# Kernel tuning notes

Hardware: AMD Instinct MI355X
Metric: run time of the kernel (lower is better)

The kernel has to match this reference:

```python
import jax, jax.numpy as jnp
import numpy as np

EPS = 1e-5

def _binarize(x):
    # binarize11: map to {-1, +1}
    return jnp.where(x >= 0, 1.0, -1.0).astype(x.dtype)

def _batchnorm(h, g, b):
    # training-mode BatchNorm1D over batch dim
    m = jnp.mean(h, axis=0)
    v = jnp.var(h, axis=0)
    return g * (h - m) * jax.lax.rsqrt(v + EPS) + b


def setup_inputs() -> dict:
    key = jax.random.key(0)
    ks = jax.random.split(key, 6)
    B = 32768
    dims = [(256, 784), (256, 256), (256, 256), (256, 256), (10, 256)]
    inp = {"x": jax.random.uniform(ks[0], (B, 784), dtype=jnp.float32)}
    for i, (o, iN) in enumerate(dims):
        inp[f"W{i}"] = jax.random.normal(ks[i + 1], (o, iN), dtype=jnp.float32)
        inp[f"g{i}"] = jnp.ones((o,), dtype=jnp.float32)
        inp[f"b{i}"] = jnp.zeros((o,), dtype=jnp.float32)
    return inp


def reference(x, W0, W1, W2, W3, W4, g0, g1, g2, g3, g4, b0, b1, b2, b3, b4):
    Ws = [W0, W1, W2, W3, W4]
    gs = [g0, g1, g2, g3, g4]
    bs = [b0, b1, b2, b3, b4]
    out = x - 0.5
    for k in range(5):
        a = _binarize(out)            # [B, in] in {-1,+1}
        wb = _binarize(Ws[k])         # [out, in] in {-1,+1}
        h = a @ wb.T                  # binary-weight linear
        out = _batchnorm(h, gs[k], bs[k])
    return jax.nn.softmax(out, axis=1)
```

## Files before the change

### kernel.cpp

```cpp
#include <hip/hip_runtime.h>
#include <stdint.h>


typedef unsigned long long u64;

#define NREP 16

#define OFF_WB0   0u
#define OFF_WB1   32768u
#define OFF_WB2   40960u
#define OFF_WB3   49152u
#define OFF_WB4   57344u
#define OFF_SUMD  57856u
#define OFF_SUMDD 139776u
#define STATS_INT4 15360
#define OFF_A1    (1u<<20)
#define OFF_A2    (2u<<20)
#define OFF_A3    (3u<<20)
#define OFF_A4    (4u<<20)
#define OFF_H0    (5u<<20)

__device__ __forceinline__ u64 pack784_sel(const float* __restrict__ src,
                                           float thr, int lane) {
  u64 w[13];
  const float4* s4 = (const float4*)src;
#pragma unroll
  for (int j = 0; j < 3; ++j) {
    float4 v = s4[j * 64 + lane];
    w[4*j+0] = __ballot(v.x >= thr);
    w[4*j+1] = __ballot(v.y >= thr);
    w[4*j+2] = __ballot(v.z >= thr);
    w[4*j+3] = __ballot(v.w >= thr);
  }
  float4 v = make_float4(-1.f, -1.f, -1.f, -1.f);
  if (lane < 4) v = s4[192 + lane];
  u64 m0 = __ballot(v.x >= thr) & 0xFull;
  u64 m1 = __ballot(v.y >= thr) & 0xFull;
  u64 m2 = __ballot(v.z >= thr) & 0xFull;
  u64 m3 = __ballot(v.w >= thr) & 0xFull;
  w[12] = m0 | (m1 << 4) | (m2 << 8) | (m3 << 12);
  u64 sel = 0;
#pragma unroll
  for (int i = 0; i < 13; ++i) sel = (lane == i) ? w[i] : sel;
  return sel;
}

__device__ __forceinline__ u64 pack256_sel(const float* __restrict__ src, int lane) {
  u64 w[4];
#pragma unroll
  for (int j = 0; j < 4; ++j) w[j] = __ballot(src[j * 64 + lane] >= 0.0f);
  u64 sel = 0;
#pragma unroll
  for (int i = 0; i < 4; ++i) sel = (lane == i) ? w[i] : sel;
  return sel;
}

__device__ __forceinline__ void bn_gs_md(const int* __restrict__ sumd_rep,
                                         const u64* __restrict__ sumdd_rep,
                                         int layer, int col,
                                         const float* __restrict__ g,
                                         float& gs, float& md_out) {
  long long sd = 0; u64 sdd = 0;
#pragma unroll
  for (int r = 0; r < NREP; ++r) {
    sd  += sumd_rep [(r * 5 + layer) * 256 + col];
    sdd += sumdd_rep[(r * 5 + layer) * 256 + col];
  }
  double md  = (double)sd  * (1.0 / 32768.0);
  double mdd = (double)sdd * (1.0 / 32768.0);
  float var = (float)(4.0 * (mdd - md * md));
  float s   = rsqrtf(var + 1e-5f);
  gs = g[col] * s;
  md_out = (float)md;
}

__global__ __launch_bounds__(256) void pack_weights(
    const float* __restrict__ W0, const float* __restrict__ W1,
    const float* __restrict__ W2, const float* __restrict__ W3,
    const float* __restrict__ W4,
    u64* __restrict__ wb0, u64* __restrict__ wb1, u64* __restrict__ wb2,
    u64* __restrict__ wb3, u64* __restrict__ wb4, int4* __restrict__ statsZ) {
  const int b = blockIdx.x, tid = threadIdx.x;
  const int lane = tid & 63, wave = tid >> 6;
  int gid = b * 256 + tid;
  if (gid < STATS_INT4) statsZ[gid] = make_int4(0, 0, 0, 0);
  if (b < 64) {
    int row = b * 4 + wave;
    u64 sel = pack784_sel(W0 + (size_t)row * 784, 0.0f, lane);
    if (lane < 13) wb0[lane * 256 + row] = sel;
  } else if (b < 128) {
    int row = (b - 64) * 4 + wave;
    u64 sel = pack256_sel(W1 + (size_t)row * 256, lane);
    if (lane < 4) wb1[lane * 256 + row] = sel;
  } else if (b < 192) {
    int row = (b - 128) * 4 + wave;
    u64 sel = pack256_sel(W2 + (size_t)row * 256, lane);
    if (lane < 4) wb2[lane * 256 + row] = sel;
  } else if (b < 256) {
    int row = (b - 192) * 4 + wave;
    u64 sel = pack256_sel(W3 + (size_t)row * 256, lane);
    if (lane < 4) wb3[lane * 256 + row] = sel;
  } else {
    for (int row = wave; row < 10; row += 4) {
      u64 sel = pack256_sel(W4 + (size_t)row * 256, lane);
      if (lane < 4) wb4[lane * 16 + row] = sel;
    }
  }
}

__global__ __launch_bounds__(256, 3) void mm0_kernel(
    const float* __restrict__ x, const u64* __restrict__ wb0T,
    short* __restrict__ h0, int* __restrict__ sumd_rep, u64* __restrict__ sumdd_rep) {
  const int b = blockIdx.x, tid = threadIdx.x;
  const int lane = tid & 63, wave = tid >> 6;
  const int row0 = b * 16;
  __shared__ u64 a0T[16 * 16];
  u64 w0  = wb0T[ 0 * 256 + tid], w1  = wb0T[ 1 * 256 + tid];
  u64 w2  = wb0T[ 2 * 256 + tid], w3  = wb0T[ 3 * 256 + tid];
  u64 w4  = wb0T[ 4 * 256 + tid], w5  = wb0T[ 5 * 256 + tid];
  u64 w6  = wb0T[ 6 * 256 + tid], w7  = wb0T[ 7 * 256 + tid];
  u64 w8  = wb0T[ 8 * 256 + tid], w9  = wb0T[ 9 * 256 + tid];
  u64 w10 = wb0T[10 * 256 + tid], w11 = wb0T[11 * 256 + tid];
  u64 w12 = wb0T[12 * 256 + tid];
  {
    const float* base = x + (size_t)(row0 + wave * 4) * 784;
#pragma unroll
    for (int it = 0; it < 4; ++it) {
      u64 sel = pack784_sel(base + (size_t)it * 784, 0.5f, lane);
      if (lane < 16) a0T[(wave * 4 + it) * 16 + lane] = sel;
    }
  }
  __syncthreads();
  int sd = 0; unsigned sdd = 0;
#pragma unroll 4
  for (int r = 0; r < 16; ++r) {
    const u64* ap = &a0T[r * 16];
    int d = __popcll(ap[0] ^ w0)   + __popcll(ap[1] ^ w1)
          + __popcll(ap[2] ^ w2)   + __popcll(ap[3] ^ w3)
          + __popcll(ap[4] ^ w4)   + __popcll(ap[5] ^ w5)
          + __popcll(ap[6] ^ w6)   + __popcll(ap[7] ^ w7)
          + __popcll(ap[8] ^ w8)   + __popcll(ap[9] ^ w9)
          + __popcll(ap[10] ^ w10) + __popcll(ap[11] ^ w11)
          + __popcll(ap[12] ^ w12);
    h0[(size_t)(row0 + r) * 256 + tid] = (short)(784 - 2 * d);
    sd += d; sdd += (unsigned)(d * d);
  }
  const int rep = b & (NREP - 1);
  atomicAdd(&sumd_rep [(rep * 5 + 0) * 256 + tid], sd);
  atomicAdd(&sumdd_rep[(rep * 5 + 0) * 256 + tid], (u64)sdd);
}

__global__ __launch_bounds__(256, 4) void b0_kernel(
    const short* __restrict__ h0,
    int* __restrict__ sumd_rep, u64* __restrict__ sumdd_rep,
    const float* __restrict__ g0, const float* __restrict__ bb0,
    u64* __restrict__ a1, const u64* __restrict__ wb1T) {
  const int b = blockIdx.x, tid = threadIdx.x;
  const int lane = tid & 63, wave = tid >> 6;
  const int row0 = b * 32;
  float gs, md;
  bn_gs_md(sumd_rep, sumdd_rep, 0, tid, g0, gs, md);
  const float mh = 784.0f - 2.0f * md;
  const float bb = bb0[tid];
  u64 wn0 = wb1T[0 * 256 + tid], wn1 = wb1T[1 * 256 + tid];
  u64 wn2 = wb1T[2 * 256 + tid], wn3 = wb1T[3 * 256 + tid];
  __shared__ u64 bits[32 * 4];
#pragma unroll 8
  for (int r = 0; r < 32; ++r) {
    float hv = (float)h0[(size_t)(row0 + r) * 256 + tid];
    bool bit = fmaf(gs, hv - mh, bb) >= 0.0f;
    u64 m = __ballot(bit);
    if (lane == 0) bits[r * 4 + wave] = m;
  }
  __syncthreads();
  if (tid < 128) a1[(size_t)row0 * 4 + tid] = bits[tid];
  int sd = 0; unsigned sdd = 0;
#pragma unroll 8
  for (int r = 0; r < 32; ++r) {
    int d = __popcll(bits[r*4+0] ^ wn0) + __popcll(bits[r*4+1] ^ wn1)
          + __popcll(bits[r*4+2] ^ wn2) + __popcll(bits[r*4+3] ^ wn3);
    sd += d; sdd += (unsigned)(d * d);
  }
  const int rep = b & (NREP - 1);
  atomicAdd(&sumd_rep [(rep * 5 + 1) * 256 + tid], sd);
  atomicAdd(&sumdd_rep[(rep * 5 + 1) * 256 + tid], (u64)sdd);
}

template<int LAYER, int NNEXT, int NSTRIDE>
__global__ __launch_bounds__(256, 4) void bmid_kernel(
    const u64* __restrict__ aK, const u64* __restrict__ wbKT,
    int* __restrict__ sumd_rep, u64* __restrict__ sumdd_rep,
    const float* __restrict__ gK, const float* __restrict__ bK,
    u64* __restrict__ aN, const u64* __restrict__ wbNT) {
  const int b = blockIdx.x, tid = threadIdx.x;
  const int lane = tid & 63, wave = tid >> 6;
  const int row0 = b * 32;
  __shared__ u64 ain[32 * 4];
  __shared__ u64 bits[32 * 4];
  if (tid < 128) ain[tid] = aK[(size_t)row0 * 4 + tid];
  float gs, md;
  bn_gs_md(sumd_rep, sumdd_rep, LAYER, tid, gK, gs, md);
  const float A = -2.0f * gs;
  const float C = fmaf(gs, 2.0f * md, bK[tid]);
  u64 wk0 = wbKT[0 * 256 + tid], wk1 = wbKT[1 * 256 + tid];
  u64 wk2 = wbKT[2 * 256 + tid], wk3 = wbKT[3 * 256 + tid];
  __syncthreads();
#pragma unroll 8
  for (int r = 0; r < 32; ++r) {
    int d = __popcll(ain[r*4+0] ^ wk0) + __popcll(ain[r*4+1] ^ wk1)
          + __popcll(ain[r*4+2] ^ wk2) + __popcll(ain[r*4+3] ^ wk3);
    bool bit = fmaf(A, (float)d, C) >= 0.0f;
    u64 m = __ballot(bit);
    if (lane == 0) bits[r * 4 + wave] = m;
  }
  __syncthreads();
  if (tid < 128) aN[(size_t)row0 * 4 + tid] = bits[tid];
  if (tid < NNEXT) {
    u64 wn0 = wbNT[0 * NSTRIDE + tid], wn1 = wbNT[1 * NSTRIDE + tid];
    u64 wn2 = wbNT[2 * NSTRIDE + tid], wn3 = wbNT[3 * NSTRIDE + tid];
    int sd = 0; unsigned sdd = 0;
#pragma unroll 8
    for (int r = 0; r < 32; ++r) {
      int d = __popcll(bits[r*4+0] ^ wn0) + __popcll(bits[r*4+1] ^ wn1)
            + __popcll(bits[r*4+2] ^ wn2) + __popcll(bits[r*4+3] ^ wn3);
      sd += d; sdd += (unsigned)(d * d);
    }
    const int rep = b & (NREP - 1);
    atomicAdd(&sumd_rep [(rep * 5 + LAYER + 1) * 256 + tid], sd);
    atomicAdd(&sumdd_rep[(rep * 5 + LAYER + 1) * 256 + tid], (u64)sdd);
  }
}

__global__ __launch_bounds__(256) void b4_kernel(
    const u64* __restrict__ a4, const u64* __restrict__ wb4T,
    const int* __restrict__ sumd_rep, const u64* __restrict__ sumdd_rep,
    const float* __restrict__ g4, const float* __restrict__ bb4,
    float* __restrict__ out) {
  __shared__ float sA[10], sC[10];
  __shared__ u64 w4s[40];
  const int tid = threadIdx.x;
  if (tid < 40) w4s[tid] = wb4T[(tid & 3) * 16 + (tid >> 2)];
  if (tid < 10) {
    float gs, md;
    bn_gs_md(sumd_rep, sumdd_rep, 4, tid, g4, gs, md);
    sA[tid] = -2.0f * gs;
    sC[tid] = fmaf(gs, 2.0f * md, bb4[tid]);
  }
  __syncthreads();
  const int row = blockIdx.x * 256 + tid;
  u64 a[4];
#pragma unroll
  for (int i = 0; i < 4; ++i) a[i] = a4[(size_t)row * 4 + i];
  float y[10];
  float mx = -1e30f;
#pragma unroll
  for (int c = 0; c < 10; ++c) {
    int d = __popcll(a[0] ^ w4s[c*4+0]) + __popcll(a[1] ^ w4s[c*4+1])
          + __popcll(a[2] ^ w4s[c*4+2]) + __popcll(a[3] ^ w4s[c*4+3]);
    y[c] = fmaf(sA[c], (float)d, sC[c]);
    mx = fmaxf(mx, y[c]);
  }
  float sum = 0.0f;
#pragma unroll
  for (int c = 0; c < 10; ++c) { y[c] = __expf(y[c] - mx); sum += y[c]; }
  float inv = 1.0f / sum;
#pragma unroll
  for (int c = 0; c < 10; ++c) out[(size_t)row * 10 + c] = y[c] * inv;
}

extern "C" void kernel_launch(void* const* d_in, const int* in_sizes, int n_in,
                              void* d_out, int out_size, void* d_ws, size_t ws_size,
                              hipStream_t stream) {
  (void)in_sizes; (void)n_in; (void)out_size; (void)ws_size;
  const float* x   = (const float*)d_in[0];
  const float* W0  = (const float*)d_in[1];
  const float* g0  = (const float*)d_in[2];
  const float* bb0 = (const float*)d_in[3];
  const float* W1  = (const float*)d_in[4];
  const float* g1  = (const float*)d_in[5];
  const float* bb1 = (const float*)d_in[6];
  const float* W2  = (const float*)d_in[7];
  const float* g2  = (const float*)d_in[8];
  const float* bb2 = (const float*)d_in[9];
  const float* W3  = (const float*)d_in[10];
  const float* g3  = (const float*)d_in[11];
  const float* bb3 = (const float*)d_in[12];
  const float* W4  = (const float*)d_in[13];
  const float* g4  = (const float*)d_in[14];
  const float* bb4 = (const float*)d_in[15];

  char* ws = (char*)d_ws;
  u64*   wb0 = (u64*)(ws + OFF_WB0);
  u64*   wb1 = (u64*)(ws + OFF_WB1);
  u64*   wb2 = (u64*)(ws + OFF_WB2);
  u64*   wb3 = (u64*)(ws + OFF_WB3);
  u64*   wb4 = (u64*)(ws + OFF_WB4);
  int*   sumd  = (int*)(ws + OFF_SUMD);
  u64*   sumdd = (u64*)(ws + OFF_SUMDD);
  u64*   a1 = (u64*)(ws + OFF_A1);
  u64*   a2 = (u64*)(ws + OFF_A2);
  u64*   a3 = (u64*)(ws + OFF_A3);
  u64*   a4 = (u64*)(ws + OFF_A4);
  short* h0 = (short*)(ws + OFF_H0);

  pack_weights<<<257, 256, 0, stream>>>(W0, W1, W2, W3, W4,
                                        wb0, wb1, wb2, wb3, wb4,
                                        (int4*)(ws + OFF_SUMD));
  mm0_kernel<<<2048, 256, 0, stream>>>(x, wb0, h0, sumd, sumdd);
  b0_kernel<<<1024, 256, 0, stream>>>(h0, sumd, sumdd, g0, bb0, a1, wb1);
  bmid_kernel<1, 256, 256><<<1024, 256, 0, stream>>>(a1, wb1, sumd, sumdd, g1, bb1, a2, wb2);
  bmid_kernel<2, 256, 256><<<1024, 256, 0, stream>>>(a2, wb2, sumd, sumdd, g2, bb2, a3, wb3);
  bmid_kernel<3, 10, 16><<<1024, 256, 0, stream>>>(a3, wb3, sumd, sumdd, g3, bb3, a4, wb4);
  b4_kernel<<<128, 256, 0, stream>>>(a4, wb4, sumd, sumdd, g4, bb4, (float*)d_out);
}
```

Baseline: 254.9 us.

## Fuse all BNN layers into one cooperative persistent kernel with grid syncs

Replaces the seven-kernel chain with a single cooperative kernel of 512 blocks, each owning 64 batch rows. Per-row popcount results stay in registers (packed 16-bit) across layers, so the intermediate activation buffers and their global traffic go away. Grid-wide syncs separate weight packing, each layer's batch-statistics accumulation, and the final softmax. The multi-kernel path is kept as a fallback if the cooperative launch fails. The risk is heavy register use under the occupancy bound needed for co-residency, and the cost of grid syncs.

```diff
diff --git a/kernel.cpp b/kernel.cpp
--- a/kernel.cpp
+++ b/kernel.cpp
@@ -1,7 +1,9 @@
 #include <hip/hip_runtime.h>
+#include <hip/hip_cooperative_groups.h>
 #include <stdint.h>
 
 
+namespace cg = cooperative_groups;
 typedef unsigned long long u64;
 
 #define NREP 16
@@ -72,6 +74,191 @@
   float s   = rsqrtf(var + 1e-5f);
   gs = g[col] * s;
   md_out = (float)md;
+}
+
+#define DPK_SET(r, d) do { if ((r) & 1) dpk[(r) >> 1] |= ((unsigned)(d)) << 16; \
+                           else dpk[(r) >> 1] = (unsigned)(d); } while (0)
+#define DPK_GET(r) ((int)((dpk[(r) >> 1] >> (((r) & 1) * 16)) & 0xFFFFu))
+
+__global__ __launch_bounds__(256, 3) void fused_bnn(
+    const float* __restrict__ x,
+    const float* __restrict__ W0, const float* __restrict__ W1,
+    const float* __restrict__ W2, const float* __restrict__ W3,
+    const float* __restrict__ W4,
+    const float* __restrict__ g0, const float* __restrict__ g1,
+    const float* __restrict__ g2, const float* __restrict__ g3,
+    const float* __restrict__ g4,
+    const float* __restrict__ bb0, const float* __restrict__ bb1,
+    const float* __restrict__ bb2, const float* __restrict__ bb3,
+    const float* __restrict__ bb4,
+    float* __restrict__ out, char* __restrict__ ws) {
+  cg::grid_group grid = cg::this_grid();
+
+  u64* wb0 = (u64*)(ws + OFF_WB0);
+  u64* wb1 = (u64*)(ws + OFF_WB1);
+  u64* wb2 = (u64*)(ws + OFF_WB2);
+  u64* wb3 = (u64*)(ws + OFF_WB3);
+  u64* wb4 = (u64*)(ws + OFF_WB4);
+  int* sumd  = (int*)(ws + OFF_SUMD);
+  u64* sumdd = (u64*)(ws + OFF_SUMDD);
+
+  const int b = blockIdx.x, tid = threadIdx.x;
+  const int lane = tid & 63, wave = tid >> 6;
+  const int row0 = b * 64;
+  const int rep = b & (NREP - 1);
+
+  __shared__ u64 aw[64 * 16];
+  __shared__ u64 bits[64 * 4];
+  __shared__ float sY[640];
+
+  unsigned dpk[32];
+
+  {
+    int gid = b * 256 + tid;
+    if (gid < STATS_INT4) ((int4*)(ws + OFF_SUMD))[gid] = make_int4(0, 0, 0, 0);
+    if (b < 64) {
+      int row = b * 4 + wave;
+      u64 sel = pack784_sel(W0 + (size_t)row * 784, 0.0f, lane);
+      if (lane < 13) wb0[lane * 256 + row] = sel;
+    } else if (b < 128) {
+      int row = (b - 64) * 4 + wave;
+      u64 sel = pack256_sel(W1 + (size_t)row * 256, lane);
+      if (lane < 4) wb1[lane * 256 + row] = sel;
+    } else if (b < 192) {
+      int row = (b - 128) * 4 + wave;
+      u64 sel = pack256_sel(W2 + (size_t)row * 256, lane);
+      if (lane < 4) wb2[lane * 256 + row] = sel;
+    } else if (b < 256) {
+      int row = (b - 192) * 4 + wave;
+      u64 sel = pack256_sel(W3 + (size_t)row * 256, lane);
+      if (lane < 4) wb3[lane * 256 + row] = sel;
+    } else if (b == 256) {
+      for (int row = wave; row < 10; row += 4) {
+        u64 sel = pack256_sel(W4 + (size_t)row * 256, lane);
+        if (lane < 4) wb4[lane * 16 + row] = sel;
+      }
+    }
+  }
+  grid.sync();
+
+  {
+    u64 w0  = wb0[ 0 * 256 + tid], w1  = wb0[ 1 * 256 + tid];
+    u64 w2  = wb0[ 2 * 256 + tid], w3  = wb0[ 3 * 256 + tid];
+    u64 w4  = wb0[ 4 * 256 + tid], w5  = wb0[ 5 * 256 + tid];
+    u64 w6  = wb0[ 6 * 256 + tid], w7  = wb0[ 7 * 256 + tid];
+    u64 w8  = wb0[ 8 * 256 + tid], w9  = wb0[ 9 * 256 + tid];
+    u64 w10 = wb0[10 * 256 + tid], w11 = wb0[11 * 256 + tid];
+    u64 w12 = wb0[12 * 256 + tid];
+    const float* base = x + (size_t)(row0 + wave * 16) * 784;
+#pragma unroll 2
+    for (int it = 0; it < 16; ++it) {
+      u64 sel = pack784_sel(base + (size_t)it * 784, 0.5f, lane);
+      if (lane < 13) aw[(wave * 16 + it) * 16 + lane] = sel;
+    }
+    __syncthreads();
+    int sd = 0; unsigned sdd = 0;
+#pragma unroll
+    for (int r = 0; r < 64; ++r) {
+      const u64* ap = &aw[r * 16];
+      int d = __popcll(ap[0] ^ w0)   + __popcll(ap[1] ^ w1)
+            + __popcll(ap[2] ^ w2)   + __popcll(ap[3] ^ w3)
+            + __popcll(ap[4] ^ w4)   + __popcll(ap[5] ^ w5)
+            + __popcll(ap[6] ^ w6)   + __popcll(ap[7] ^ w7)
+            + __popcll(ap[8] ^ w8)   + __popcll(ap[9] ^ w9)
+            + __popcll(ap[10] ^ w10) + __popcll(ap[11] ^ w11)
+            + __popcll(ap[12] ^ w12);
+      DPK_SET(r, d);
+      sd += d; sdd += (unsigned)(d * d);
+    }
+    atomicAdd(&sumd [(rep * 5 + 0) * 256 + tid], sd);
+    atomicAdd(&sumdd[(rep * 5 + 0) * 256 + tid], (u64)sdd);
+  }
+  grid.sync();
+
+#pragma unroll
+  for (int k = 0; k < 3; ++k) {
+    const float* gk  = (k == 0) ? g0  : (k == 1) ? g1  : g2;
+    const float* bk  = (k == 0) ? bb0 : (k == 1) ? bb1 : bb2;
+    const u64*   wbN = (k == 0) ? wb1 : (k == 1) ? wb2 : wb3;
+    float gs, md;
+    bn_gs_md(sumd, sumdd, k, tid, gk, gs, md);
+    const float A = -2.0f * gs;
+    const float C = fmaf(gs, 2.0f * md, bk[tid]);
+#pragma unroll
+    for (int r = 0; r < 64; ++r) {
+      bool bit = fmaf(A, (float)DPK_GET(r), C) >= 0.0f;
+      u64 m = __ballot(bit);
+      if (lane == 0) bits[r * 4 + wave] = m;
+    }
+    __syncthreads();
+    u64 wn0 = wbN[0 * 256 + tid], wn1 = wbN[1 * 256 + tid];
+    u64 wn2 = wbN[2 * 256 + tid], wn3 = wbN[3 * 256 + tid];
+    int sd = 0; unsigned sdd = 0;
+#pragma unroll
+    for (int r = 0; r < 64; ++r) {
+      int d = __popcll(bits[r*4+0] ^ wn0) + __popcll(bits[r*4+1] ^ wn1)
+            + __popcll(bits[r*4+2] ^ wn2) + __popcll(bits[r*4+3] ^ wn3);
+      DPK_SET(r, d);
+      sd += d; sdd += (unsigned)(d * d);
+    }
+    atomicAdd(&sumd [(rep * 5 + k + 1) * 256 + tid], sd);
+    atomicAdd(&sumdd[(rep * 5 + k + 1) * 256 + tid], (u64)sdd);
+    grid.sync();
+  }
+
+  {
+    float gs, md;
+    bn_gs_md(sumd, sumdd, 3, tid, g3, gs, md);
+    const float A = -2.0f * gs;
+    const float C = fmaf(gs, 2.0f * md, bb3[tid]);
+#pragma unroll
+    for (int r = 0; r < 64; ++r) {
+      bool bit = fmaf(A, (float)DPK_GET(r), C) >= 0.0f;
+      u64 m = __ballot(bit);
+      if (lane == 0) bits[r * 4 + wave] = m;
+    }
+    __syncthreads();
+    if (tid < 10) {
+      u64 wn0 = wb4[0 * 16 + tid], wn1 = wb4[1 * 16 + tid];
+      u64 wn2 = wb4[2 * 16 + tid], wn3 = wb4[3 * 16 + tid];
+      int sd = 0; unsigned sdd = 0;
+#pragma unroll
+      for (int r = 0; r < 64; ++r) {
+        int d = __popcll(bits[r*4+0] ^ wn0) + __popcll(bits[r*4+1] ^ wn1)
+              + __popcll(bits[r*4+2] ^ wn2) + __popcll(bits[r*4+3] ^ wn3);
+        DPK_SET(r, d);
+        sd += d; sdd += (unsigned)(d * d);
+      }
+      atomicAdd(&sumd [(rep * 5 + 4) * 256 + tid], sd);
+      atomicAdd(&sumdd[(rep * 5 + 4) * 256 + tid], (u64)sdd);
+    }
+  }
+  grid.sync();
+
+  {
+    if (tid < 10) {
+      float gs, md;
+      bn_gs_md(sumd, sumdd, 4, tid, g4, gs, md);
+      const float A = -2.0f * gs;
+      const float C = fmaf(gs, 2.0f * md, bb4[tid]);
+#pragma unroll
+      for (int r = 0; r < 64; ++r)
+        sY[r * 10 + tid] = fmaf(A, (float)DPK_GET(r), C);
+    }
+    __syncthreads();
+    if (tid < 64) {
+      float y[10]; float mx = -1e30f;
+#pragma unroll
+      for (int c = 0; c < 10; ++c) { y[c] = sY[tid * 10 + c]; mx = fmaxf(mx, y[c]); }
+      float sum = 0.0f;
+#pragma unroll
+      for (int c = 0; c < 10; ++c) { y[c] = __expf(y[c] - mx); sum += y[c]; }
+      float inv = 1.0f / sum;
+      float* op = out + (size_t)(row0 + tid) * 10;
+#pragma unroll
+      for (int c = 0; c < 10; ++c) op[c] = y[c] * inv;
+    }
+  }
 }
 
 __global__ __launch_bounds__(256) void pack_weights(
@@ -288,28 +475,38 @@
   const float* W4  = (const float*)d_in[13];
   const float* g4  = (const float*)d_in[14];
   const float* bb4 = (const float*)d_in[15];
-
+  float* outp = (float*)d_out;
   char* ws = (char*)d_ws;
-  u64*   wb0 = (u64*)(ws + OFF_WB0);
-  u64*   wb1 = (u64*)(ws + OFF_WB1);
-  u64*   wb2 = (u64*)(ws + OFF_WB2);
-  u64*   wb3 = (u64*)(ws + OFF_WB3);
-  u64*   wb4 = (u64*)(ws + OFF_WB4);
-  int*   sumd  = (int*)(ws + OFF_SUMD);
-  u64*   sumdd = (u64*)(ws + OFF_SUMDD);
-  u64*   a1 = (u64*)(ws + OFF_A1);
-  u64*   a2 = (u64*)(ws + OFF_A2);
-  u64*   a3 = (u64*)(ws + OFF_A3);
-  u64*   a4 = (u64*)(ws + OFF_A4);
-  short* h0 = (short*)(ws + OFF_H0);
-
-  pack_weights<<<257, 256, 0, stream>>>(W0, W1, W2, W3, W4,
-                                        wb0, wb1, wb2, wb3, wb4,
-                                        (int4*)(ws + OFF_SUMD));
-  mm0_kernel<<<2048, 256, 0, stream>>>(x, wb0, h0, sumd, sumdd);
-  b0_kernel<<<1024, 256, 0, stream>>>(h0, sumd, sumdd, g0, bb0, a1, wb1);
-  bmid_kernel<1, 256, 256><<<1024, 256, 0, stream>>>(a1, wb1, sumd, sumdd, g1, bb1, a2, wb2);
-  bmid_kernel<2, 256, 256><<<1024, 256, 0, stream>>>(a2, wb2, sumd, sumdd, g2, bb2, a3, wb3);
-  bmid_kernel<3, 10, 16><<<1024, 256, 0, stream>>>(a3, wb3, sumd, sumdd, g3, bb3, a4, wb4);
-  b4_kernel<<<128, 256, 0, stream>>>(a4, wb4, sumd, sumdd, g4, bb4, (float*)d_out);
-}
+
+  void* args[] = { &x, &W0, &W1, &W2, &W3, &W4,
+                   &g0, &g1, &g2, &g3, &g4,
+                   &bb0, &bb1, &bb2, &bb3, &bb4,
+                   &outp, &ws };
+  hipError_t err = hipLaunchCooperativeKernel((const void*)fused_bnn,
+                                              dim3(512), dim3(256),
+                                              args, 0, stream);
+  if (err != hipSuccess) {
+    (void)hipGetLastError();
+    u64*   wb0 = (u64*)(ws + OFF_WB0);
+    u64*   wb1 = (u64*)(ws + OFF_WB1);
+    u64*   wb2 = (u64*)(ws + OFF_WB2);
+    u64*   wb3 = (u64*)(ws + OFF_WB3);
+    u64*   wb4 = (u64*)(ws + OFF_WB4);
+    int*   sumd  = (int*)(ws + OFF_SUMD);
+    u64*   sumdd = (u64*)(ws + OFF_SUMDD);
+    u64*   a1 = (u64*)(ws + OFF_A1);
+    u64*   a2 = (u64*)(ws + OFF_A2);
+    u64*   a3 = (u64*)(ws + OFF_A3);
+    u64*   a4 = (u64*)(ws + OFF_A4);
+    short* h0 = (short*)(ws + OFF_H0);
+    pack_weights<<<257, 256, 0, stream>>>(W0, W1, W2, W3, W4,
+                                          wb0, wb1, wb2, wb3, wb4,
+                                          (int4*)(ws + OFF_SUMD));
+    mm0_kernel<<<2048, 256, 0, stream>>>(x, wb0, h0, sumd, sumdd);
+    b0_kernel<<<1024, 256, 0, stream>>>(h0, sumd, sumdd, g0, bb0, a1, wb1);
+    bmid_kernel<1, 256, 256><<<1024, 256, 0, stream>>>(a1, wb1, sumd, sumdd, g1, bb1, a2, wb2);
+    bmid_kernel<2, 256, 256><<<1024, 256, 0, stream>>>(a2, wb2, sumd, sumdd, g2, bb2, a3, wb3);
+    bmid_kernel<3, 10, 16><<<1024, 256, 0, stream>>>(a3, wb3, sumd, sumdd, g3, bb3, a4, wb4);
+    b4_kernel<<<128, 256, 0, stream>>>(a4, wb4, sumd, sumdd, g4, bb4, (float*)d_out);
+  }
+}
```

After: 579.2 us. +127.2%, slower.

## Fuse all BNN layers into one persistent kernel with grid barriers

Applied to the files above, without the earlier changes.

Replaces the six per-layer kernels with a single persistent kernel of 512 blocks, each owning 64 rows. Per-row popcount results stay packed in registers across layers, so the intermediate h0 and activation bit arrays no longer go through global memory. BatchNorm statistics are synchronised with a hierarchical atomic grid barrier. In exchange it relies on all 512 blocks being co-resident, where a spin barrier could deadlock if they are not. It also raises register pressure, and the final layers leave most threads idle.

```diff
diff --git a/kernel.cpp b/kernel.cpp
--- a/kernel.cpp
+++ b/kernel.cpp
@@ -5,6 +5,9 @@
 typedef unsigned long long u64;
 
 #define NREP 16
+#define GRID_BLOCKS 512
+#define NGROUPS 32
+#define GROUP_SZ 16
 
 #define OFF_WB0   0u
 #define OFF_WB1   32768u
@@ -13,12 +16,8 @@
 #define OFF_WB4   57344u
 #define OFF_SUMD  57856u
 #define OFF_SUMDD 139776u
-#define STATS_INT4 15360
-#define OFF_A1    (1u<<20)
-#define OFF_A2    (2u<<20)
-#define OFF_A3    (3u<<20)
-#define OFF_A4    (4u<<20)
-#define OFF_H0    (5u<<20)
+#define OFF_BAR   303616u
+#define ZERO_INT4 16144
 
 __device__ __forceinline__ u64 pack784_sel(const float* __restrict__ src,
                                            float thr, int lane) {
@@ -63,8 +62,10 @@
   long long sd = 0; u64 sdd = 0;
 #pragma unroll
   for (int r = 0; r < NREP; ++r) {
-    sd  += sumd_rep [(r * 5 + layer) * 256 + col];
-    sdd += sumdd_rep[(r * 5 + layer) * 256 + col];
+    sd  += __hip_atomic_load(&sumd_rep [(r * 5 + layer) * 256 + col],
+                             __ATOMIC_RELAXED, __HIP_MEMORY_SCOPE_AGENT);
+    sdd += __hip_atomic_load(&sumdd_rep[(r * 5 + layer) * 256 + col],
+                             __ATOMIC_RELAXED, __HIP_MEMORY_SCOPE_AGENT);
   }
   double md  = (double)sd  * (1.0 / 32768.0);
   double mdd = (double)sdd * (1.0 / 32768.0);
@@ -74,16 +75,55 @@
   md_out = (float)md;
 }
 
+#define DPK_SET(r, d) do { if ((r) & 1) dpk[(r) >> 1] |= ((unsigned)(d)) << 16; \
+                           else dpk[(r) >> 1] = (unsigned)(d); } while (0)
+#define DPK_GET(r) ((int)((dpk[(r) >> 1] >> (((r) & 1) * 16)) & 0xFFFFu))
+
+__device__ __forceinline__ void stats_add(int* pd, u64* pdd, int sd, u64 sdd) {
+  int o1 = atomicAdd(pd, sd);
+  u64 o2 = atomicAdd(pdd, sdd);
+  asm volatile("" :: "v"(o1), "v"(o2));
+}
+
+__device__ __forceinline__ void grid_barrier(unsigned* bar, unsigned phase, int b) {
+  __syncthreads();
+  if (threadIdx.x == 0) {
+    asm volatile("s_waitcnt vmcnt(0)" ::: "memory");
+    const unsigned g = (unsigned)b >> 4;
+    unsigned a = __hip_atomic_fetch_add(&bar[g * 64], 1u, __ATOMIC_RELAXED,
+                                        __HIP_MEMORY_SCOPE_AGENT) + 1u;
+    bool released = false;
+    if (a == phase * GROUP_SZ) {
+      unsigned r = __hip_atomic_fetch_add(&bar[32 * 64], 1u, __ATOMIC_RELAXED,
+                                          __HIP_MEMORY_SCOPE_AGENT) + 1u;
+      if (r == phase * NGROUPS) {
+#pragma unroll
+        for (int i = 0; i < 16; ++i)
+          __hip_atomic_store(&bar[(33 + i) * 64], phase, __ATOMIC_RELAXED,
+                             __HIP_MEMORY_SCOPE_AGENT);
+        released = true;
+      }
+    }
+    if (!released) {
+      const unsigned* genp = &bar[(33 + (b & 15)) * 64];
+      while (__hip_atomic_load(genp, __ATOMIC_RELAXED,
+                               __HIP_MEMORY_SCOPE_AGENT) < phase)
+        __builtin_amdgcn_s_sleep(8);
+    }
+  }
+  __syncthreads();
+}
+
 __global__ __launch_bounds__(256) void pack_weights(
     const float* __restrict__ W0, const float* __restrict__ W1,
     const float* __restrict__ W2, const float* __restrict__ W3,
     const float* __restrict__ W4,
     u64* __restrict__ wb0, u64* __restrict__ wb1, u64* __restrict__ wb2,
-    u64* __restrict__ wb3, u64* __restrict__ wb4, int4* __restrict__ statsZ) {
+    u64* __restrict__ wb3, u64* __restrict__ wb4, int4* __restrict__ zeroRgn) {
   const int b = blockIdx.x, tid = threadIdx.x;
   const int lane = tid & 63, wave = tid >> 6;
   int gid = b * 256 + tid;
-  if (gid < STATS_INT4) statsZ[gid] = make_int4(0, 0, 0, 0);
+  if (gid < ZERO_INT4) zeroRgn[gid] = make_int4(0, 0, 0, 0);
   if (b < 64) {
     int row = b * 4 + wave;
     u64 sel = pack784_sel(W0 + (size_t)row * 784, 0.0f, lane);
@@ -108,164 +148,153 @@
   }
 }
 
-__global__ __launch_bounds__(256, 3) void mm0_kernel(
-    const float* __restrict__ x, const u64* __restrict__ wb0T,
-    short* __restrict__ h0, int* __restrict__ sumd_rep, u64* __restrict__ sumdd_rep) {
+__global__ __launch_bounds__(256, 3) void fused_bnn(
+    const float* __restrict__ x,
+    const float* __restrict__ g0, const float* __restrict__ g1,
+    const float* __restrict__ g2, const float* __restrict__ g3,
+    const float* __restrict__ g4,
+    const float* __restrict__ bb0, const float* __restrict__ bb1,
+    const float* __restrict__ bb2, const float* __restrict__ bb3,
+    const float* __restrict__ bb4,
+    float* __restrict__ out, char* __restrict__ ws) {
+  u64* wb0 = (u64*)(ws + OFF_WB0);
+  u64* wb1 = (u64*)(ws + OFF_WB1);
+  u64* wb2 = (u64*)(ws + OFF_WB2);
+  u64* wb3 = (u64*)(ws + OFF_WB3);
+  u64* wb4 = (u64*)(ws + OFF_WB4);
+  int* sumd  = (int*)(ws + OFF_SUMD);
+  u64* sumdd = (u64*)(ws + OFF_SUMDD);
+  unsigned* bar = (unsigned*)(ws + OFF_BAR);
+
   const int b = blockIdx.x, tid = threadIdx.x;
   const int lane = tid & 63, wave = tid >> 6;
-  const int row0 = b * 16;
-  __shared__ u64 a0T[16 * 16];
-  u64 w0  = wb0T[ 0 * 256 + tid], w1  = wb0T[ 1 * 256 + tid];
-  u64 w2  = wb0T[ 2 * 256 + tid], w3  = wb0T[ 3 * 256 + tid];
-  u64 w4  = wb0T[ 4 * 256 + tid], w5  = wb0T[ 5 * 256 + tid];
-  u64 w6  = wb0T[ 6 * 256 + tid], w7  = wb0T[ 7 * 256 + tid];
-  u64 w8  = wb0T[ 8 * 256 + tid], w9  = wb0T[ 9 * 256 + tid];
-  u64 w10 = wb0T[10 * 256 + tid], w11 = wb0T[11 * 256 + tid];
-  u64 w12 = wb0T[12 * 256 + tid];
+  const int row0 = b * 64;
+  const int rep = b & (NREP - 1);
+
+  __shared__ u64 aw[64 * 16];
+  __shared__ u64 bits[64 * 4];
+  __shared__ float sY[640];
+
+  unsigned dpk[32];
+
   {
-    const float* base = x + (size_t)(row0 + wave * 4) * 784;
-#pragma unroll
-    for (int it = 0; it < 4; ++it) {
+    u64 w0  = wb0[ 0 * 256 + tid], w1  = wb0[ 1 * 256 + tid];
+    u64 w2  = wb0[ 2 * 256 + tid], w3  = wb0[ 3 * 256 + tid];
+    u64 w4  = wb0[ 4 * 256 + tid], w5  = wb0[ 5 * 256 + tid];
+    u64 w6  = wb0[ 6 * 256 + tid], w7  = wb0[ 7 * 256 + tid];
+    u64 w8  = wb0[ 8 * 256 + tid], w9  = wb0[ 9 * 256 + tid];
+    u64 w10 = wb0[10 * 256 + tid], w11 = wb0[11 * 256 + tid];
+    u64 w12 = wb0[12 * 256 + tid];
+    const float* base = x + (size_t)(row0 + wave * 16) * 784;
+#pragma unroll 2
+    for (int it = 0; it < 16; ++it) {
       u64 sel = pack784_sel(base + (size_t)it * 784, 0.5f, lane);
-      if (lane < 16) a0T[(wave * 4 + it) * 16 + lane] = sel;
-    }
-  }
-  __syncthreads();
-  int sd = 0; unsigned sdd = 0;
-#pragma unroll 4
-  for (int r = 0; r < 16; ++r) {
-    const u64* ap = &a0T[r * 16];
-    int d = __popcll(ap[0] ^ w0)   + __popcll(ap[1] ^ w1)
-          + __popcll(ap[2] ^ w2)   + __popcll(ap[3] ^ w3)
-          + __popcll(ap[4] ^ w4)   + __popcll(ap[5] ^ w5)
-          + __popcll(ap[6] ^ w6)   + __popcll(ap[7] ^ w7)
-          + __popcll(ap[8] ^ w8)   + __popcll(ap[9] ^ w9)
-          + __popcll(ap[10] ^ w10) + __popcll(ap[11] ^ w11)
-          + __popcll(ap[12] ^ w12);
-    h0[(size_t)(row0 + r) * 256 + tid] = (short)(784 - 2 * d);
-    sd += d; sdd += (unsigned)(d * d);
-  }
-  const int rep = b & (NREP - 1);
-  atomicAdd(&sumd_rep [(rep * 5 + 0) * 256 + tid], sd);
-  atomicAdd(&sumdd_rep[(rep * 5 + 0) * 256 + tid], (u64)sdd);
-}
-
-__global__ __launch_bounds__(256, 4) void b0_kernel(
-    const short* __restrict__ h0,
-    int* __restrict__ sumd_rep, u64* __restrict__ sumdd_rep,
-    const float* __restrict__ g0, const float* __restrict__ bb0,
-    u64* __restrict__ a1, const u64* __restrict__ wb1T) {
-  const int b = blockIdx.x, tid = threadIdx.x;
-  const int lane = tid & 63, wave = tid >> 6;
-  const int row0 = b * 32;
-  float gs, md;
-  bn_gs_md(sumd_rep, sumdd_rep, 0, tid, g0, gs, md);
-  const float mh = 784.0f - 2.0f * md;
-  const float bb = bb0[tid];
-  u64 wn0 = wb1T[0 * 256 + tid], wn1 = wb1T[1 * 256 + tid];
-  u64 wn2 = wb1T[2 * 256 + tid], wn3 = wb1T[3 * 256 + tid];
-  __shared__ u64 bits[32 * 4];
-#pragma unroll 8
-  for (int r = 0; r < 32; ++r) {
-    float hv = (float)h0[(size_t)(row0 + r) * 256 + tid];
-    bool bit = fmaf(gs, hv - mh, bb) >= 0.0f;
-    u64 m = __ballot(bit);
-    if (lane == 0) bits[r * 4 + wave] = m;
-  }
-  __syncthreads();
-  if (tid < 128) a1[(size_t)row0 * 4 + tid] = bits[tid];
-  int sd = 0; unsigned sdd = 0;
-#pragma unroll 8
-  for (int r = 0; r < 32; ++r) {
-    int d = __popcll(bits[r*4+0] ^ wn0) + __popcll(bits[r*4+1] ^ wn1)
-          + __popcll(bits[r*4+2] ^ wn2) + __popcll(bits[r*4+3] ^ wn3);
-    sd += d; sdd += (unsigned)(d * d);
-  }
-  const int rep = b & (NREP - 1);
-  atomicAdd(&sumd_rep [(rep * 5 + 1) * 256 + tid], sd);
-  atomicAdd(&sumdd_rep[(rep * 5 + 1) * 256 + tid], (u64)sdd);
-}
-
-template<int LAYER, int NNEXT, int NSTRIDE>
-__global__ __launch_bounds__(256, 4) void bmid_kernel(
-    const u64* __restrict__ aK, const u64* __restrict__ wbKT,
-    int* __restrict__ sumd_rep, u64* __restrict__ sumdd_rep,
-    const float* __restrict__ gK, const float* __restrict__ bK,
-    u64* __restrict__ aN, const u64* __restrict__ wbNT) {
-  const int b = blockIdx.x, tid = threadIdx.x;
-  const int lane = tid & 63, wave = tid >> 6;
-  const int row0 = b * 32;
-  __shared__ u64 ain[32 * 4];
-  __shared__ u64 bits[32 * 4];
-  if (tid < 128) ain[tid] = aK[(size_t)row0 * 4 + tid];
-  float gs, md;
-  bn_gs_md(sumd_rep, sumdd_rep, LAYER, tid, gK, gs, md);
-  const float A = -2.0f * gs;
-  const float C = fmaf(gs, 2.0f * md, bK[tid]);
-  u64 wk0 = wbKT[0 * 256 + tid], wk1 = wbKT[1 * 256 + tid];
-  u64 wk2 = wbKT[2 * 256 + tid], wk3 = wbKT[3 * 256 + tid];
-  __syncthreads();
-#pragma unroll 8
-  for (int r = 0; r < 32; ++r) {
-    int d = __popcll(ain[r*4+0] ^ wk0) + __popcll(ain[r*4+1] ^ wk1)
-          + __popcll(ain[r*4+2] ^ wk2) + __popcll(ain[r*4+3] ^ wk3);
-    bool bit = fmaf(A, (float)d, C) >= 0.0f;
-    u64 m = __ballot(bit);
-    if (lane == 0) bits[r * 4 + wave] = m;
-  }
-  __syncthreads();
-  if (tid < 128) aN[(size_t)row0 * 4 + tid] = bits[tid];
-  if (tid < NNEXT) {
-    u64 wn0 = wbNT[0 * NSTRIDE + tid], wn1 = wbNT[1 * NSTRIDE + tid];
-    u64 wn2 = wbNT[2 * NSTRIDE + tid], wn3 = wbNT[3 * NSTRIDE + tid];
+      if (lane < 13) aw[(wave * 16 + it) * 16 + lane] = sel;
+    }
+    __syncthreads();
     int sd = 0; unsigned sdd = 0;
-#pragma unroll 8
-    for (int r = 0; r < 32; ++r) {
+#pragma unroll
+    for (int r = 0; r < 64; ++r) {
+      const u64* ap = &aw[r * 16];
+      int d = __popcll(ap[0] ^ w0)   + __popcll(ap[1] ^ w1)
+            + __popcll(ap[2] ^ w2)   + __popcll(ap[3] ^ w3)
+            + __popcll(ap[4] ^ w4)   + __popcll(ap[5] ^ w5)
+            + __popcll(ap[6] ^ w6)   + __popcll(ap[7] ^ w7)
+            + __popcll(ap[8] ^ w8)   + __popcll(ap[9] ^ w9)
+            + __popcll(ap[10] ^ w10) + __popcll(ap[11] ^ w11)
+            + __popcll(ap[12] ^ w12);
+      DPK_SET(r, d);
+      sd += d; sdd += (unsigned)(d * d);
+    }
+    stats_add(&sumd[(rep * 5 + 0) * 256 + tid],
+              &sumdd[(rep * 5 + 0) * 256 + tid], sd, (u64)sdd);
+  }
+  grid_barrier(bar, 1, b);
+
+#pragma unroll
+  for (int k = 0; k < 3; ++k) {
+    const float* gk  = (k == 0) ? g0  : (k == 1) ? g1  : g2;
+    const float* bk  = (k == 0) ? bb0 : (k == 1) ? bb1 : bb2;
+    const u64*   wbN = (k == 0) ? wb1 : (k == 1) ? wb2 : wb3;
+    float gs, md;
+    bn_gs_md(sumd, sumdd, k, tid, gk, gs, md);
+    const float A = -2.0f * gs;
+    const float C = fmaf(gs, 2.0f * md, bk[tid]);
+#pragma unroll
+    for (int r = 0; r < 64; ++r) {
+      bool bit = fmaf(A, (float)DPK_GET(r), C) >= 0.0f;
+      u64 m = __ballot(bit);
+      if (lane == 0) bits[r * 4 + wave] = m;
+    }
+    __syncthreads();
+    u64 wn0 = wbN[0 * 256 + tid], wn1 = wbN[1 * 256 + tid];
+    u64 wn2 = wbN[2 * 256 + tid], wn3 = wbN[3 * 256 + tid];
+    int sd = 0; unsigned sdd = 0;
+#pragma unroll
+    for (int r = 0; r < 64; ++r) {
       int d = __popcll(bits[r*4+0] ^ wn0) + __popcll(bits[r*4+1] ^ wn1)
             + __popcll(bits[r*4+2] ^ wn2) + __popcll(bits[r*4+3] ^ wn3);
+      DPK_SET(r, d);
       sd += d; sdd += (unsigned)(d * d);
     }
-    const int rep = b & (NREP - 1);
-    atomicAdd(&sumd_rep [(rep * 5 + LAYER + 1) * 256 + tid], sd);
-    atomicAdd(&sumdd_rep[(rep * 5 + LAYER + 1) * 256 + tid], (u64)sdd);
-  }
-}
-
-__global__ __launch_bounds__(256) void b4_kernel(
-    const u64* __restrict__ a4, const u64* __restrict__ wb4T,
-    const int* __restrict__ sumd_rep, const u64* __restrict__ sumdd_rep,
-    const float* __restrict__ g4, const float* __restrict__ bb4,
-    float* __restrict__ out) {
-  __shared__ float sA[10], sC[10];
-  __shared__ u64 w4s[40];
-  const int tid = threadIdx.x;
-  if (tid < 40) w4s[tid] = wb4T[(tid & 3) * 16 + (tid >> 2)];
-  if (tid < 10) {
+    stats_add(&sumd[(rep * 5 + k + 1) * 256 + tid],
+              &sumdd[(rep * 5 + k + 1) * 256 + tid], sd, (u64)sdd);
+    grid_barrier(bar, 2 + k, b);
+  }
+
+  {
     float gs, md;
-    bn_gs_md(sumd_rep, sumdd_rep, 4, tid, g4, gs, md);
-    sA[tid] = -2.0f * gs;
-    sC[tid] = fmaf(gs, 2.0f * md, bb4[tid]);
-  }
-  __syncthreads();
-  const int row = blockIdx.x * 256 + tid;
-  u64 a[4];
-#pragma unroll
-  for (int i = 0; i < 4; ++i) a[i] = a4[(size_t)row * 4 + i];
-  float y[10];
-  float mx = -1e30f;
-#pragma unroll
-  for (int c = 0; c < 10; ++c) {
-    int d = __popcll(a[0] ^ w4s[c*4+0]) + __popcll(a[1] ^ w4s[c*4+1])
-          + __popcll(a[2] ^ w4s[c*4+2]) + __popcll(a[3] ^ w4s[c*4+3]);
-    y[c] = fmaf(sA[c], (float)d, sC[c]);
-    mx = fmaxf(mx, y[c]);
-  }
-  float sum = 0.0f;
-#pragma unroll
-  for (int c = 0; c < 10; ++c) { y[c] = __expf(y[c] - mx); sum += y[c]; }
-  float inv = 1.0f / sum;
-#pragma unroll
-  for (int c = 0; c < 10; ++c) out[(size_t)row * 10 + c] = y[c] * inv;
+    bn_gs_md(sumd, sumdd, 3, tid, g3, gs, md);
+    const float A = -2.0f * gs;
+    const float C = fmaf(gs, 2.0f * md, bb3[tid]);
+#pragma unroll
+    for (int r = 0; r < 64; ++r) {
+      bool bit = fmaf(A, (float)DPK_GET(r), C) >= 0.0f;
+      u64 m = __ballot(bit);
+      if (lane == 0) bits[r * 4 + wave] = m;
+    }
+    __syncthreads();
+    if (tid < 10) {
+      u64 wn0 = wb4[0 * 16 + tid], wn1 = wb4[1 * 16 + tid];
+      u64 wn2 = wb4[2 * 16 + tid], wn3 = wb4[3 * 16 + tid];
+      int sd = 0; unsigned sdd = 0;
+#pragma unroll
+      for (int r = 0; r < 64; ++r) {
+        int d = __popcll(bits[r*4+0] ^ wn0) + __popcll(bits[r*4+1] ^ wn1)
+              + __popcll(bits[r*4+2] ^ wn2) + __popcll(bits[r*4+3] ^ wn3);
+        DPK_SET(r, d);
+        sd += d; sdd += (unsigned)(d * d);
+      }
+      stats_add(&sumd[(rep * 5 + 4) * 256 + tid],
+                &sumdd[(rep * 5 + 4) * 256 + tid], sd, (u64)sdd);
+    }
+  }
+  grid_barrier(bar, 5, b);
+
+  {
+    if (tid < 10) {
+      float gs, md;
+      bn_gs_md(sumd, sumdd, 4, tid, g4, gs, md);
+      const float A = -2.0f * gs;
+      const float C = fmaf(gs, 2.0f * md, bb4[tid]);
+#pragma unroll
+      for (int r = 0; r < 64; ++r)
+        sY[r * 10 + tid] = fmaf(A, (float)DPK_GET(r), C);
+    }
+    __syncthreads();
+    if (tid < 64) {
+      float y[10]; float mx = -1e30f;
+#pragma unroll
+      for (int c = 0; c < 10; ++c) { y[c] = sY[tid * 10 + c]; mx = fmaxf(mx, y[c]); }
+      float sum = 0.0f;
+#pragma unroll
+      for (int c = 0; c < 10; ++c) { y[c] = __expf(y[c] - mx); sum += y[c]; }
+      float inv = 1.0f / sum;
+      float* op = out + (size_t)(row0 + tid) * 10;
+#pragma unroll
+      for (int c = 0; c < 10; ++c) op[c] = y[c] * inv;
+    }
+  }
 }
 
 extern "C" void kernel_launch(void* const* d_in, const int* in_sizes, int n_in,
@@ -288,28 +317,18 @@
   const float* W4  = (const float*)d_in[13];
   const float* g4  = (const float*)d_in[14];
   const float* bb4 = (const float*)d_in[15];
-
   char* ws = (char*)d_ws;
-  u64*   wb0 = (u64*)(ws + OFF_WB0);
-  u64*   wb1 = (u64*)(ws + OFF_WB1);
-  u64*   wb2 = (u64*)(ws + OFF_WB2);
-  u64*   wb3 = (u64*)(ws + OFF_WB3);
-  u64*   wb4 = (u64*)(ws + OFF_WB4);
-  int*   sumd  = (int*)(ws + OFF_SUMD);
-  u64*   sumdd = (u64*)(ws + OFF_SUMDD);
-  u64*   a1 = (u64*)(ws + OFF_A1);
-  u64*   a2 = (u64*)(ws + OFF_A2);
-  u64*   a3 = (u64*)(ws + OFF_A3);
-  u64*   a4 = (u64*)(ws + OFF_A4);
-  short* h0 = (short*)(ws + OFF_H0);
+
+  u64* wb0 = (u64*)(ws + OFF_WB0);
+  u64* wb1 = (u64*)(ws + OFF_WB1);
+  u64* wb2 = (u64*)(ws + OFF_WB2);
+  u64* wb3 = (u64*)(ws + OFF_WB3);
+  u64* wb4 = (u64*)(ws + OFF_WB4);
 
   pack_weights<<<257, 256, 0, stream>>>(W0, W1, W2, W3, W4,
                                         wb0, wb1, wb2, wb3, wb4,
                                         (int4*)(ws + OFF_SUMD));
-  mm0_kernel<<<2048, 256, 0, stream>>>(x, wb0, h0, sumd, sumdd);
-  b0_kernel<<<1024, 256, 0, stream>>>(h0, sumd, sumdd, g0, bb0, a1, wb1);
-  bmid_kernel<1, 256, 256><<<1024, 256, 0, stream>>>(a1, wb1, sumd, sumdd, g1, bb1, a2, wb2);
-  bmid_kernel<2, 256, 256><<<1024, 256, 0, stream>>>(a2, wb2, sumd, sumdd, g2, bb2, a3, wb3);
-  bmid_kernel<3, 10, 16><<<1024, 256, 0, stream>>>(a3, wb3, sumd, sumdd, g3, bb3, a4, wb4);
-  b4_kernel<<<128, 256, 0, stream>>>(a4, wb4, sumd, sumdd, g4, bb4, (float*)d_out);
-}
+  fused_bnn<<<GRID_BLOCKS, 256, 0, stream>>>(
+      x, g0, g1, g2, g3, g4, bb0, bb1, bb2, bb3, bb4,
+      (float*)d_out, ws);
+}
```

After: 269.8 us. +5.8%, slower.
